# Optimization experiments

Measured on AMD Instinct MI355X. Metric: run time of the kernel, lower is better.

## Reference

```python
import jax, jax.numpy as jnp
import numpy as np

N_EXPERTS = 8
D_MODEL = 1024
D_FFN = 4096
BLOCK_SIZE = 2048
N_EXPERT_CAPACITY = 2
BATCH = 4
K = BLOCK_SIZE * N_EXPERT_CAPACITY // N_EXPERTS  # 512 tokens per expert


def setup_inputs() -> dict:
    key = jax.random.key(0)
    k1, k2, k3, k4 = jax.random.split(key, 4)
    x = jax.random.normal(k1, (BATCH, BLOCK_SIZE, D_MODEL), dtype=jnp.float32)
    # kaiming-uniform-like scales: bound = 1/sqrt(fan_in)
    choice = jax.random.uniform(k2, (N_EXPERTS, D_MODEL), minval=-1.0, maxval=1.0) / np.sqrt(D_MODEL)
    w1 = jax.random.uniform(k3, (N_EXPERTS, D_FFN, D_MODEL), minval=-1.0, maxval=1.0) / np.sqrt(D_MODEL)
    w2 = jax.random.uniform(k4, (N_EXPERTS, D_MODEL, D_FFN), minval=-1.0, maxval=1.0) / np.sqrt(D_FFN)
    return {"x": x, "choice": choice.astype(jnp.float32), "w1": w1.astype(jnp.float32), "w2": w2.astype(jnp.float32)}


def reference(x, choice, w1, w2):
    # expert-choice routing: each expert picks top-K tokens
    logits = jnp.einsum('bsd,ed->bse', x, choice)          # [b,s,e]
    probs = jax.nn.softmax(logits, axis=-1)
    G, I = jax.lax.top_k(jnp.swapaxes(probs, -1, -2), K)   # [b,e,k] gates, token ids
    P = jax.nn.one_hot(I, BLOCK_SIZE, dtype=x.dtype)       # [b,e,k,s] one-hot dispatch
    # dispatch tokens to experts
    x_in = jnp.einsum('beks,bsd->bekd', P, x)              # [b,e,k,d]
    # per-expert SwiGLU-style FFN (silu(x W1^T) W2^T)
    h = jax.nn.silu(jnp.einsum('beki,eoi->beko', x_in, w1))  # [b,e,k,d_ffn]
    x_mlp = jnp.einsum('beki,eoi->beko', h, w2)              # [b,e,k,d_model]
    # scatter back to token slots per expert, then combine with gates
    x_e = jnp.einsum('beks,bekd->besd', P, x_mlp)          # [b,e,s,d]
    x_out = jnp.einsum('beks,bek,besd->bsd', P, G, x_e)    # [b,s,d]
    return x_out
```

## Files before the change

kernel.cpp:

```cpp
#include <hip/hip_runtime.h>
#include <stdint.h>

#define B_   4
#define S_   2048
#define D_   1024
#define F_   4096
#define E_   8
#define KSEL 512

typedef __attribute__((ext_vector_type(8))) short short8;
typedef __attribute__((ext_vector_type(4))) float floatx4;

__device__ __forceinline__ unsigned short f2bf(float f) {
    unsigned u = __float_as_uint(f);
    unsigned r = (u + 0x7FFFu + ((u >> 16) & 1u)) >> 16;
    return (unsigned short)r;
}

__device__ __forceinline__ void gload16(const void* g, void* l) {
    __builtin_amdgcn_global_load_lds(
        (const __attribute__((address_space(1))) void*)g,
        (__attribute__((address_space(3))) void*)l, 16, 0, 0);
}

__device__ __forceinline__ void barw()     { asm volatile("s_barrier" ::: "memory"); }
__device__ __forceinline__ void wait_vm8() { asm volatile("s_waitcnt vmcnt(8)" ::: "memory"); }
__device__ __forceinline__ void wait_vm0() { asm volatile("s_waitcnt vmcnt(0)" ::: "memory"); }

__global__ void convert_kernel(const float* __restrict__ src,
                               unsigned short* __restrict__ dst, int n4) {
    int i = blockIdx.x * blockDim.x + threadIdx.x;
    int stride = gridDim.x * blockDim.x;
    const float4* s4 = (const float4*)src;
    ushort4* d4 = (ushort4*)dst;
    for (; i < n4; i += stride) {
        float4 v = s4[i];
        ushort4 o;
        o.x = f2bf(v.x); o.y = f2bf(v.y); o.z = f2bf(v.z); o.w = f2bf(v.w);
        d4[i] = o;
    }
}

__global__ void router_kernel(const float* __restrict__ x,
                              const float* __restrict__ choice,
                              float* __restrict__ probs,
                              unsigned short* __restrict__ xb) {
    int bs = blockIdx.x;
    int b = bs >> 11, s = bs & 2047;
    int tid = threadIdx.x;
    const float4* xr = (const float4*)(x + (size_t)bs * D_);
    float4 xv = xr[tid];
    ushort4 o;
    o.x = f2bf(xv.x); o.y = f2bf(xv.y); o.z = f2bf(xv.z); o.w = f2bf(xv.w);
    ((ushort4*)(xb + (size_t)bs * D_))[tid] = o;

    float acc[E_];
#pragma unroll
    for (int e = 0; e < E_; e++) {
        const float4* cr = (const float4*)(choice + e * D_);
        float4 cv = cr[tid];
        acc[e] = xv.x * cv.x + xv.y * cv.y + xv.z * cv.z + xv.w * cv.w;
    }
    __shared__ float red[E_][4];
    int lane = tid & 63, w = tid >> 6;
#pragma unroll
    for (int e = 0; e < E_; e++) {
        float v = acc[e];
        for (int off = 32; off; off >>= 1) v += __shfl_down(v, off, 64);
        if (lane == 0) red[e][w] = v;
    }
    __syncthreads();
    if (tid == 0) {
        float l[E_], m = -1e30f;
#pragma unroll
        for (int e = 0; e < E_; e++) {
            l[e] = red[e][0] + red[e][1] + red[e][2] + red[e][3];
            m = fmaxf(m, l[e]);
        }
        float sum = 0.f, p[E_];
#pragma unroll
        for (int e = 0; e < E_; e++) { p[e] = __expf(l[e] - m); sum += p[e]; }
        float inv = 1.0f / sum;
#pragma unroll
        for (int e = 0; e < E_; e++)
            probs[((size_t)b * E_ + e) * S_ + s] = p[e] * inv;
    }
}

__global__ void topk_kernel(const float* __restrict__ probs,
                            int* __restrict__ idxb, float* __restrict__ gateb) {
    __shared__ float ps[S_];
    int be = blockIdx.x >> 3;
    int chunk = blockIdx.x & 7;
    const float* p = probs + (size_t)be * S_;
    for (int i = threadIdx.x; i < S_; i += 256) ps[i] = p[i];
    __syncthreads();
    int t = chunk * 256 + threadIdx.x;
    float pt = ps[t];
    int rank = 0;
    for (int s = 0; s < S_; s++) {
        float v = ps[s];
        rank += (v > pt) || (v == pt && s < t);
    }
    if (rank < KSEL) {
        idxb[be * KSEL + rank] = t;
        gateb[be * KSEL + rank] = pt;
    }
}

template<int MH, int NH>
__device__ __forceinline__ void mfma_quad(const short8 (&af)[4][2], const short8 (&bf)[2][2],
                                          floatx4 (&acc)[8][4]) {
#pragma unroll
    for (int ks = 0; ks < 2; ++ks)
#pragma unroll
        for (int m2 = 0; m2 < 4; ++m2)
#pragma unroll
            for (int n2 = 0; n2 < 2; ++n2)
                acc[MH*4+m2][NH*2+n2] = __builtin_amdgcn_mfma_f32_16x16x32_bf16(
                    af[m2][ks], bf[n2][ks], acc[MH*4+m2][NH*2+n2], 0, 0, 0);
}

template<int NK>
__device__ __forceinline__ void mm_core(const char* const aS[4], const char* const bS[4],
                                        char* smem, int tid, floatx4 (&acc)[8][4]) {
    const int lane = tid & 63;
    const int wid  = tid >> 6;
    const int wm   = wid >> 2;
    const int wn   = wid & 3;
    const int mrow = lane & 15;
    const int hi   = lane >> 4;
    const int sw0  = (hi ^ (mrow & 7)) << 4;
    const int sw1  = ((hi + 4) ^ (mrow & 7)) << 4;
    const int arow = (wm * 128 + mrow) * 128;
    const int brow = 32768 + (wn * 64 + mrow) * 128;

    int dstA[4], dstB[4];
#pragma unroll
    for (int q = 0; q < 2; ++q)
#pragma unroll
        for (int r = 0; r < 2; ++r) {
            dstA[q*2+r] = q * 8192 + r * 16384 + tid * 16;
            dstB[q*2+r] = 32768 + ((tid >> 8) + 2*r) * 8192 + q * 4096 + (tid & 255) * 16;
        }

    short8 af[4][2], bf0[2][2], bf1[2][2];

#define STG_A(P,Q,K) { gload16(aS[(Q)*2+0] + (size_t)(K)*128, smem + (P)*65536 + dstA[(Q)*2+0]); \
                       gload16(aS[(Q)*2+1] + (size_t)(K)*128, smem + (P)*65536 + dstA[(Q)*2+1]); }
#define STG_B(P,Q,K) { gload16(bS[(Q)*2+0] + (size_t)(K)*128, smem + (P)*65536 + dstB[(Q)*2+0]); \
                       gload16(bS[(Q)*2+1] + (size_t)(K)*128, smem + (P)*65536 + dstB[(Q)*2+1]); }

    STG_A(0,0,0); STG_B(0,0,0); STG_B(0,1,0); STG_A(0,1,0);
    STG_A(1,0,1); STG_B(1,0,1); STG_B(1,1,1); STG_A(1,1,1);
    wait_vm8();
    barw();

    for (int kt = 0; kt < NK; ++kt) {
        const int p  = kt & 1;
        const int k2 = (kt + 2) & (NK - 1);
        const char* bA = smem + p * 65536;

#pragma unroll
        for (int m2 = 0; m2 < 4; ++m2) {
            const char* rb = bA + arow + m2 * 2048;
            af[m2][0] = *(const short8*)(rb + sw0);
            af[m2][1] = *(const short8*)(rb + sw1);
        }
#pragma unroll
        for (int n2 = 0; n2 < 2; ++n2) {
            const char* rb = bA + brow + n2 * 2048;
            bf0[n2][0] = *(const short8*)(rb + sw0);
            bf0[n2][1] = *(const short8*)(rb + sw1);
        }
        barw();
        __builtin_amdgcn_s_setprio(1);
        mfma_quad<0,0>(af, bf0, acc);
        __builtin_amdgcn_s_setprio(0);
        barw();

#pragma unroll
        for (int n2 = 0; n2 < 2; ++n2) {
            const char* rb = bA + brow + (2 + n2) * 2048;
            bf1[n2][0] = *(const short8*)(rb + sw0);
            bf1[n2][1] = *(const short8*)(rb + sw1);
        }
        STG_A(p, 0, k2);
        barw();
        __builtin_amdgcn_s_setprio(1);
        mfma_quad<0,1>(af, bf1, acc);
        __builtin_amdgcn_s_setprio(0);
        barw();

#pragma unroll
        for (int m2 = 0; m2 < 4; ++m2) {
            const char* rb = bA + arow + (4 + m2) * 2048;
            af[m2][0] = *(const short8*)(rb + sw0);
            af[m2][1] = *(const short8*)(rb + sw1);
        }
        STG_B(p, 0, k2);
        barw();
        __builtin_amdgcn_s_setprio(1);
        mfma_quad<1,1>(af, bf1, acc);
        __builtin_amdgcn_s_setprio(0);
        barw();

        STG_B(p, 1, k2);
        STG_A(p, 1, k2);
        wait_vm8();
        barw();
        __builtin_amdgcn_s_setprio(1);
        mfma_quad<1,0>(af, bf0, acc);
        __builtin_amdgcn_s_setprio(0);
        barw();
    }
    wait_vm0();
#undef STG_A
#undef STG_B
}

__global__ __launch_bounds__(512) void gemm1_8ph(
    const unsigned short* __restrict__ xb, const unsigned short* __restrict__ w1b,
    const int* __restrict__ idxb, unsigned short* __restrict__ hbuf) {
    extern __shared__ __align__(16) char smem[];
    const int tid = threadIdx.x;
    const int blk = blockIdx.x;
    const int e  = blk & 7;
    const int q  = blk >> 3;
    const int b  = q >> 5;
    const int tm = (q >> 4) & 1;
    const int tn = q & 15;
    const int g  = b * 8 + e;

    const int t8   = tid >> 3;
    const int cswz = ((tid & 7) ^ (t8 & 7)) << 4;

    const char* aS[4]; const char* bS[4];
    {
        const int ar[4] = { t8, 128 + t8, 64 + t8, 192 + t8 };
#pragma unroll
        for (int i = 0; i < 4; ++i) {
            int tok = idxb[g * KSEL + tm * 256 + ar[i]];
            aS[i] = (const char*)xb + ((size_t)(b * S_ + tok) * D_) * 2 + cswz;
        }
        const int u = tid >> 8, v = t8 & 31;
#pragma unroll
        for (int qq = 0; qq < 2; ++qq)
#pragma unroll
            for (int r = 0; r < 2; ++r) {
                int rowb = (u + 2*r) * 64 + qq * 32 + v;
                bS[qq*2+r] = (const char*)w1b + ((size_t)(e * F_ + tn * 256 + rowb) * D_) * 2 + cswz;
            }
    }

    floatx4 acc[8][4];
#pragma unroll
    for (int m = 0; m < 8; ++m)
#pragma unroll
        for (int n = 0; n < 4; ++n) acc[m][n] = (floatx4){0.f, 0.f, 0.f, 0.f};

    mm_core<D_ / 64>(aS, bS, smem, tid, acc);

    const int lane = tid & 63, wid = tid >> 6;
    const int wm = wid >> 2, wn = wid & 3;
    const int mrow = lane & 15, hi = lane >> 4;
    unsigned short* hr = hbuf + (size_t)g * ((size_t)KSEL * F_);
#pragma unroll
    for (int m = 0; m < 8; ++m) {
#pragma unroll
        for (int r2 = 0; r2 < 4; ++r2) {
            const int rowc = tm*256 + wm*128 + m*16 + hi*4 + r2;
            unsigned short* hrow = hr + (size_t)rowc * F_ + tn*256 + wn*64 + mrow;
#pragma unroll
            for (int n = 0; n < 4; ++n) {
                float v = acc[m][n][r2];
                float s = v / (1.0f + __expf(-v));
                hrow[n * 16] = f2bf(s);
            }
        }
    }
}

__global__ __launch_bounds__(512) void gemm2_8ph(
    const unsigned short* __restrict__ hbuf, const unsigned short* __restrict__ w2b,
    const int* __restrict__ idxb, const float* __restrict__ gateb,
    float* __restrict__ out) {
    extern __shared__ __align__(16) char smem[];
    const int tid = threadIdx.x;
    const int blk = blockIdx.x;
    const int e  = blk & 7;
    const int q  = blk >> 3;
    const int b  = q >> 3;
    const int tm = (q >> 2) & 1;
    const int tn = q & 3;
    const int g  = b * 8 + e;

    const int t8   = tid >> 3;
    const int cswz = ((tid & 7) ^ (t8 & 7)) << 4;

    const char* aS[4]; const char* bS[4];
    {
        const int ar[4] = { t8, 128 + t8, 64 + t8, 192 + t8 };
#pragma unroll
        for (int i = 0; i < 4; ++i)
            aS[i] = (const char*)hbuf + ((size_t)(g * KSEL + tm * 256 + ar[i]) * F_) * 2 + cswz;
        const int u = tid >> 8, v = t8 & 31;
#pragma unroll
        for (int qq = 0; qq < 2; ++qq)
#pragma unroll
            for (int r = 0; r < 2; ++r) {
                int rowb = (u + 2*r) * 64 + qq * 32 + v;
                bS[qq*2+r] = (const char*)w2b + ((size_t)(e * D_ + tn * 256 + rowb) * F_) * 2 + cswz;
            }
    }

    floatx4 acc[8][4];
#pragma unroll
    for (int m = 0; m < 8; ++m)
#pragma unroll
        for (int n = 0; n < 4; ++n) acc[m][n] = (floatx4){0.f, 0.f, 0.f, 0.f};

    mm_core<F_ / 64>(aS, bS, smem, tid, acc);

    const int lane = tid & 63, wid = tid >> 6;
    const int wm = wid >> 2, wn = wid & 3;
    const int mrow = lane & 15, hi = lane >> 4;
#pragma unroll
    for (int m = 0; m < 8; ++m) {
#pragma unroll
        for (int r2 = 0; r2 < 4; ++r2) {
            const int slot = tm*256 + wm*128 + m*16 + hi*4 + r2;
            const int tok  = idxb[g * KSEL + slot];
            const float gt = gateb[g * KSEL + slot];
            float* orow = out + ((size_t)b * S_ + tok) * D_ + tn*256 + wn*64 + mrow;
#pragma unroll
            for (int n = 0; n < 4; ++n)
                atomicAdd(&orow[n * 16], gt * acc[m][n][r2]);
        }
    }
}

extern "C" void kernel_launch(void* const* d_in, const int* in_sizes, int n_in,
                              void* d_out, int out_size, void* d_ws, size_t ws_size,
                              hipStream_t stream) {
    const float* x      = (const float*)d_in[0];
    const float* choice = (const float*)d_in[1];
    const float* w1     = (const float*)d_in[2];
    const float* w2     = (const float*)d_in[3];
    float* out = (float*)d_out;
    char* ws = (char*)d_ws;

    static bool inited = false;
    if (!inited) {
        hipFuncSetAttribute(reinterpret_cast<const void*>(&gemm1_8ph),
                            hipFuncAttributeMaxDynamicSharedMemorySize, 131072);
        hipFuncSetAttribute(reinterpret_cast<const void*>(&gemm2_8ph),
                            hipFuncAttributeMaxDynamicSharedMemorySize, 131072);
        inited = true;
    }

    unsigned short* w1b = (unsigned short*)(ws);
    unsigned short* w2b = (unsigned short*)(ws + 67108864);
    unsigned short* xb  = (unsigned short*)(ws + 134217728);
    unsigned short* hb  = (unsigned short*)(ws + 150994944);
    float* probs        = (float*)(ws + 285212672);
    int*   idxb         = (int*)(ws + 285474816);
    float* gateb        = (float*)(ws + 285540352);

    hipMemsetAsync(d_out, 0, (size_t)out_size * sizeof(float), stream);
    convert_kernel<<<8192, 256, 0, stream>>>(w1, w1b, 8388608);
    convert_kernel<<<8192, 256, 0, stream>>>(w2, w2b, 8388608);
    router_kernel<<<B_ * S_, 256, 0, stream>>>(x, choice, probs, xb);
    topk_kernel<<<B_ * E_ * 8, 256, 0, stream>>>(probs, idxb, gateb);
    gemm1_8ph<<<1024, 512, 131072, stream>>>(xb, w1b, idxb, hb);
    gemm2_8ph<<<256, 512, 131072, stream>>>(hb, w2b, idxb, gateb, out);
}
```

Measured before the change: 696.6 us.

## Replace atomic scatter-add with per-slot stores and gather-based combine kernel

The second GEMM now writes gate-scaled expert outputs with plain stores into a per-slot buffer, reusing the bf16 W1 workspace after the first GEMM has finished with it. It no longer does float atomicAdds into the output. Top-k builds a per-token list of the expert slots that chose each token, and a new combine kernel sums those rows into the output, so the output memset is no longer needed. The two weight conversions are also merged into one launch. The gain is removing scattered atomic contention, at the cost of an extra 64 MB intermediate write and read plus one more kernel launch.

```diff
diff --git a/kernel.cpp b/kernel.cpp
--- a/kernel.cpp
+++ b/kernel.cpp
@@ -27,24 +27,28 @@
 __device__ __forceinline__ void wait_vm8() { asm volatile("s_waitcnt vmcnt(8)" ::: "memory"); }
 __device__ __forceinline__ void wait_vm0() { asm volatile("s_waitcnt vmcnt(0)" ::: "memory"); }
 
-__global__ void convert_kernel(const float* __restrict__ src,
-                               unsigned short* __restrict__ dst, int n4) {
+__global__ void convert2_kernel(const float* __restrict__ s0, unsigned short* __restrict__ d0,
+                                const float* __restrict__ s1, unsigned short* __restrict__ d1,
+                                int n4) {
     int i = blockIdx.x * blockDim.x + threadIdx.x;
     int stride = gridDim.x * blockDim.x;
-    const float4* s4 = (const float4*)src;
-    ushort4* d4 = (ushort4*)dst;
-    for (; i < n4; i += stride) {
-        float4 v = s4[i];
+    for (; i < 2 * n4; i += stride) {
+        const int sel = i < n4;
+        const float4* s4 = (const float4*)(sel ? s0 : s1);
+        ushort4* d4 = (ushort4*)(sel ? d0 : d1);
+        const int j = sel ? i : i - n4;
+        float4 v = s4[j];
         ushort4 o;
         o.x = f2bf(v.x); o.y = f2bf(v.y); o.z = f2bf(v.z); o.w = f2bf(v.w);
-        d4[i] = o;
+        d4[j] = o;
     }
 }
 
 __global__ void router_kernel(const float* __restrict__ x,
                               const float* __restrict__ choice,
                               float* __restrict__ probs,
-                              unsigned short* __restrict__ xb) {
+                              unsigned short* __restrict__ xb,
+                              int* __restrict__ cnt) {
     int bs = blockIdx.x;
     int b = bs >> 11, s = bs & 2047;
     int tid = threadIdx.x;
@@ -71,6 +75,7 @@
     }
     __syncthreads();
     if (tid == 0) {
+        cnt[bs] = 0;
         float l[E_], m = -1e30f;
 #pragma unroll
         for (int e = 0; e < E_; e++) {
@@ -88,7 +93,8 @@
 }
 
 __global__ void topk_kernel(const float* __restrict__ probs,
-                            int* __restrict__ idxb, float* __restrict__ gateb) {
+                            int* __restrict__ idxb, float* __restrict__ gateb,
+                            int* __restrict__ cnt, int* __restrict__ lst) {
     __shared__ float ps[S_];
     int be = blockIdx.x >> 3;
     int chunk = blockIdx.x & 7;
@@ -105,6 +111,9 @@
     if (rank < KSEL) {
         idxb[be * KSEL + rank] = t;
         gateb[be * KSEL + rank] = pt;
+        int b = be >> 3;
+        int pos = atomicAdd(&cnt[b * S_ + t], 1);
+        lst[(b * S_ + t) * 8 + pos] = be * KSEL + rank;
     }
 }
 
@@ -283,8 +292,7 @@
 
 __global__ __launch_bounds__(512) void gemm2_8ph(
     const unsigned short* __restrict__ hbuf, const unsigned short* __restrict__ w2b,
-    const int* __restrict__ idxb, const float* __restrict__ gateb,
-    float* __restrict__ out) {
+    const float* __restrict__ gateb, float* __restrict__ cmb) {
     extern __shared__ __align__(16) char smem[];
     const int tid = threadIdx.x;
     const int blk = blockIdx.x;
@@ -330,14 +338,29 @@
 #pragma unroll
         for (int r2 = 0; r2 < 4; ++r2) {
             const int slot = tm*256 + wm*128 + m*16 + hi*4 + r2;
-            const int tok  = idxb[g * KSEL + slot];
             const float gt = gateb[g * KSEL + slot];
-            float* orow = out + ((size_t)b * S_ + tok) * D_ + tn*256 + wn*64 + mrow;
+            float* crow = cmb + ((size_t)g * KSEL + slot) * D_ + tn*256 + wn*64 + mrow;
 #pragma unroll
             for (int n = 0; n < 4; ++n)
-                atomicAdd(&orow[n * 16], gt * acc[m][n][r2]);
-        }
-    }
+                crow[n * 16] = gt * acc[m][n][r2];
+        }
+    }
+}
+
+__global__ void combine_kernel(const float* __restrict__ cmb,
+                               const int* __restrict__ cnt,
+                               const int* __restrict__ lst,
+                               float* __restrict__ out) {
+    const int bs = blockIdx.x;
+    const int tid = threadIdx.x;
+    const int c = cnt[bs];
+    float4 acc = {0.f, 0.f, 0.f, 0.f};
+    for (int i = 0; i < c; ++i) {
+        const int idx = lst[bs * 8 + i];
+        const float4 v = ((const float4*)(cmb + (size_t)idx * D_))[tid];
+        acc.x += v.x; acc.y += v.y; acc.z += v.z; acc.w += v.w;
+    }
+    ((float4*)(out + (size_t)bs * D_))[tid] = acc;
 }
 
 extern "C" void kernel_launch(void* const* d_in, const int* in_sizes, int n_in,
@@ -366,12 +389,14 @@
     float* probs        = (float*)(ws + 285212672);
     int*   idxb         = (int*)(ws + 285474816);
     float* gateb        = (float*)(ws + 285540352);
-
-    hipMemsetAsync(d_out, 0, (size_t)out_size * sizeof(float), stream);
-    convert_kernel<<<8192, 256, 0, stream>>>(w1, w1b, 8388608);
-    convert_kernel<<<8192, 256, 0, stream>>>(w2, w2b, 8388608);
-    router_kernel<<<B_ * S_, 256, 0, stream>>>(x, choice, probs, xb);
-    topk_kernel<<<B_ * E_ * 8, 256, 0, stream>>>(probs, idxb, gateb);
+    int*   cnt          = (int*)(ws + 285605888);
+    int*   lst          = (int*)(ws + 285638656);
+    float* cmb          = (float*)(ws);
+
+    convert2_kernel<<<16384, 256, 0, stream>>>(w1, w1b, w2, w2b, 8388608);
+    router_kernel<<<B_ * S_, 256, 0, stream>>>(x, choice, probs, xb, cnt);
+    topk_kernel<<<B_ * E_ * 8, 256, 0, stream>>>(probs, idxb, gateb, cnt, lst);
     gemm1_8ph<<<1024, 512, 131072, stream>>>(xb, w1b, idxb, hb);
-    gemm2_8ph<<<256, 512, 131072, stream>>>(hb, w2b, idxb, gateb, out);
-}
+    gemm2_8ph<<<256, 512, 131072, stream>>>(hb, w2b, gateb, cmb);
+    combine_kernel<<<B_ * S_, 256, 0, stream>>>(cmb, cnt, lst, out);
+}
```

Result: faster. 662.1 us (-4.9%).
